# Kernel optimization log

Hardware: AMD Instinct MI355X
Metric: run time of the kernel (lower is better)

The kernel has to match this reference:

```python
import jax, jax.numpy as jnp
import numpy as np

N_EMBED = 1024
N_HEADS = 16


def setup_inputs() -> dict:
    key = jax.random.key(0)
    k_x, k_wa, k_wp = jax.random.split(key, 3)
    B, T, C = 2, 2048, N_EMBED
    x = jax.random.normal(k_x, (B, T, C), dtype=jnp.float32)
    # flax Dense default: lecun_normal kernel, zero bias; use scaled normal here
    w_attn = jax.random.normal(k_wa, (C, 3 * C), dtype=jnp.float32) / np.sqrt(C)
    b_attn = jnp.zeros((3 * C,), dtype=jnp.float32)
    w_proj = jax.random.normal(k_wp, (C, C), dtype=jnp.float32) / np.sqrt(C)
    b_proj = jnp.zeros((C,), dtype=jnp.float32)
    return {"x": x, "w_attn": w_attn, "b_attn": b_attn,
            "w_proj": w_proj, "b_proj": b_proj}


def reference(x, w_attn, b_attn, w_proj, b_proj):
    B, T, C = x.shape
    H = N_HEADS
    D = C // H
    qkv = x @ w_attn + b_attn                      # [B,T,3C]
    q, k, v = jnp.split(qkv, 3, axis=-1)           # each [B,T,C]
    q = q.reshape(B, T, H, D).swapaxes(1, 2)       # [B,H,T,D]
    k = k.reshape(B, T, H, D).swapaxes(1, 2)
    v = v.reshape(B, T, H, D).swapaxes(1, 2)
    att = jnp.einsum('bhid,bhjd->bhij', q, k) * (1.0 / jnp.sqrt(D))
    causal = jnp.tril(jnp.ones((T, T), dtype=bool))
    att = jnp.where(causal, att, -jnp.inf)
    att = jax.nn.softmax(att, axis=-1)
    y = jnp.einsum('bhij,bhjd->bhid', att, v)      # [B,H,T,D]
    y = y.swapaxes(1, 2).reshape(B, T, C)
    return y @ w_proj + b_proj
```

## Files before the change

kernel.cpp:

```cpp
#include <hip/hip_runtime.h>
#include <hip/hip_bf16.h>

typedef __bf16 bf16x8 __attribute__((ext_vector_type(8)));
typedef float f32x4 __attribute__((ext_vector_type(4)));
typedef float f32x16 __attribute__((ext_vector_type(16)));
typedef unsigned short u16;
typedef unsigned int u32;
typedef u16 u16x8 __attribute__((ext_vector_type(8)));
typedef u32 u32x4 __attribute__((ext_vector_type(4)));

#define SM_SCALE 0.1803368801111244f

#define FEXP2(x) __builtin_amdgcn_exp2f(x)
#define FLOG2(x) __builtin_amdgcn_logf(x)

__device__ inline u16 tobf(float f) {
  u32 u = __builtin_bit_cast(u32, f);
  u32 r = (u + 0x7fffu + ((u >> 16) & 1u)) >> 16;
  return (u16)r;
}

__device__ inline float frombf(u16 h) {
  return __builtin_bit_cast(float, (u32)h << 16);
}

__device__ inline void gload_lds16(const void* g, void* lds) {
  __builtin_amdgcn_global_load_lds(
      (const __attribute__((address_space(1))) u32*)g,
      (__attribute__((address_space(3))) u32*)lds, 16, 0, 0);
}

template <int N>
__device__ __forceinline__ void wait_vmcnt() {
  if constexpr (N == 0)
    asm volatile("s_waitcnt vmcnt(0)" ::: "memory");
  else if constexpr (N == 5)
    asm volatile("s_waitcnt vmcnt(5)" ::: "memory");
  else if constexpr (N == 7)
    asm volatile("s_waitcnt vmcnt(7)" ::: "memory");
}

__device__ __forceinline__ void transpose_body(const float* __restrict__ in,
                                               u16* __restrict__ out, int K,
                                               int N, int bxg, int tid) {
  __shared__ float tile[32][33];
  int nbx = N >> 5;
  int bx = bxg % nbx, by = bxg / nbx;
  int k0 = by << 5, n0 = bx << 5;
  int tx = tid & 31, ty = tid >> 5;
#pragma unroll
  for (int j = 0; j < 4; ++j) {
    int row = ty + j * 8;
    tile[row][tx] = in[(size_t)(k0 + row) * N + n0 + tx];
  }
  __syncthreads();
#pragma unroll
  for (int j = 0; j < 4; ++j) {
    int row = ty + j * 8;
    out[(size_t)(n0 + row) * K + k0 + tx] = tobf(tile[tx][row]);
  }
}

__global__ __launch_bounds__(256) void prep_kernel(
    const float* __restrict__ x, u16* __restrict__ xb,
    const float* __restrict__ wa, u16* __restrict__ wat,
    const float* __restrict__ wp, u16* __restrict__ wpt) {
  const int b = blockIdx.x, tid = threadIdx.x;
  if (b < 2048) {
    int i = b * 256 + tid;
    const float4* p = (const float4*)x + (size_t)i * 2;
    float4 a = p[0], c = p[1];
    u16x8 v;
    v[0] = tobf(a.x); v[1] = tobf(a.y); v[2] = tobf(a.z); v[3] = tobf(a.w);
    v[4] = tobf(c.x); v[5] = tobf(c.y); v[6] = tobf(c.z); v[7] = tobf(c.w);
    *(u16x8*)(xb + (size_t)i * 8) = v;
  } else if (b < 5120) {
    transpose_body(wa, wat, 1024, 3072, b - 2048, tid);
  } else {
    transpose_body(wp, wpt, 1024, 1024, b - 5120, tid);
  }
}

template <int EPI, int BN>
__global__ __launch_bounds__(256) void gemm_bt(
    const u16* __restrict__ A, const u16* __restrict__ Bt,
    const float* __restrict__ bias,
    u16* __restrict__ o0, u16* __restrict__ o1, u16* __restrict__ o2,
    float* __restrict__ fo, int M, int N, int K) {
  constexpr int NF = BN / 32;
  __shared__ __align__(16) u16 As[2][128 * 64];
  __shared__ __align__(16) u16 Bs[2][BN * 64];
  const int tid = threadIdx.x;
  const int lane = tid & 63;
  const int wave = tid >> 6;
  const int nbn = N / BN;
  int bid = (int)blockIdx.x;
  const int cpx = (int)gridDim.x >> 3;
  bid = (bid & 7) * cpx + (bid >> 3);
  const int bm = bid / nbn, bn = bid % nbn;
  const int m0 = bm << 7, n0 = bn * BN;
  const int wr = wave >> 1, wc = wave & 1;
  const int r15 = lane & 15, g = lane >> 4;

  f32x4 acc[4][NF] = {};

#define GSTAGE(buf, kt)                                                    \
  do {                                                                     \
    _Pragma("unroll")                                                      \
    for (int j = 0; j < 4; ++j) {                                          \
      int c = j * 4 + wave;                                                \
      int byte0 = c * 1024 + lane * 16;                                    \
      int row = byte0 >> 7;                                                \
      int colb = (byte0 & 127) ^ ((row & 7) << 4);                         \
      gload_lds16(A + (size_t)(m0 + row) * K + (kt) * 64 + (colb >> 1),    \
                  (char*)As[(buf)] + c * 1024);                            \
    }                                                                      \
    _Pragma("unroll")                                                      \
    for (int j = 0; j < NF; ++j) {                                         \
      int c = j * 4 + wave;                                                \
      int byte0 = c * 1024 + lane * 16;                                    \
      int row = byte0 >> 7;                                                \
      int colb = (byte0 & 127) ^ ((row & 7) << 4);                         \
      gload_lds16(Bt + (size_t)(n0 + row) * K + (kt) * 64 + (colb >> 1),   \
                  (char*)Bs[(buf)] + c * 1024);                            \
    }                                                                      \
  } while (0)

  const int nkt = K >> 6;
  GSTAGE(0, 0);
  for (int kt = 0; kt < nkt; ++kt) {
    const int cur = kt & 1;
    if (kt + 1 < nkt) {
      GSTAGE(cur ^ 1, kt + 1);
      wait_vmcnt<4 + NF>();
    } else {
      wait_vmcnt<0>();
    }
    __builtin_amdgcn_s_barrier();
#pragma unroll
    for (int kk = 0; kk < 2; ++kk) {
      bf16x8 af[4], bf[NF];
#pragma unroll
      for (int i = 0; i < 4; ++i) {
        int rowA = wr * 64 + i * 16 + r15;
        int ca = (kk * 64 + 16 * g) ^ ((rowA & 7) << 4);
        af[i] = *(const bf16x8*)((const char*)As[cur] + rowA * 128 + ca);
      }
#pragma unroll
      for (int j2 = 0; j2 < NF; ++j2) {
        int rowB = wc * (BN / 2) + j2 * 16 + r15;
        int cb = (kk * 64 + 16 * g) ^ ((rowB & 7) << 4);
        bf[j2] = *(const bf16x8*)((const char*)Bs[cur] + rowB * 128 + cb);
      }
#pragma unroll
      for (int i = 0; i < 4; ++i)
#pragma unroll
        for (int j2 = 0; j2 < NF; ++j2)
          acc[i][j2] = __builtin_amdgcn_mfma_f32_16x16x32_bf16(
              af[i], bf[j2], acc[i][j2], 0, 0, 0);
    }
    if (kt + 1 < nkt) __builtin_amdgcn_s_barrier();
  }
#undef GSTAGE

#pragma unroll
  for (int j2 = 0; j2 < NF; ++j2) {
    const int n = n0 + wc * (BN / 2) + j2 * 16 + r15;
    const float bv = bias[n];
#pragma unroll
    for (int i = 0; i < 4; ++i) {
      const int mb = m0 + wr * 64 + i * 16 + g * 4;
      float v[4];
#pragma unroll
      for (int rr = 0; rr < 4; ++rr) v[rr] = acc[i][j2][rr] + bv;
      if (EPI == 1) {
#pragma unroll
        for (int rr = 0; rr < 4; ++rr) fo[(size_t)(mb + rr) * N + n] = v[rr];
      } else {
        const int b = mb >> 11, t = mb & 2047;
        const int sec = n >> 10, nn = n & 1023;
        const int h = nn >> 6, d = nn & 63;
        const int bh = b * 16 + h;
        if (sec == 0) {
          u16* base = o0 + ((size_t)bh * 2048 + t) * 64 + d;
#pragma unroll
          for (int rr = 0; rr < 4; ++rr) base[rr * 64] = tobf(v[rr] * SM_SCALE);
        } else if (sec == 1) {
          u16* kb = o1 +
                    (((size_t)(bh * 32 + (t >> 6)) * 4 + (d >> 4)) * 2) * 512 +
                    ((d >> 3) & 1) * 256 + (d & 7);
          const int tb = t & 63;
#pragma unroll
          for (int rr = 0; rr < 4; ++rr) {
            int r = tb + rr;
            kb[(r >> 5) * 512 + (r & 31) * 8] = tobf(v[rr]);
          }
        } else {
          const int tl = t & 63;
          u16* vb = o2 +
                    ((((size_t)(bh * 32 + (t >> 6)) * 4 + (tl >> 4)) * 2 +
                      (d >> 5)) * 512) +
                    ((tl >> 3) & 1) * 256 + (d & 31) * 8 + (tl & 7);
          u32* p = (u32*)vb;
          p[0] = (u32)tobf(v[0]) | ((u32)tobf(v[1]) << 16);
          p[1] = (u32)tobf(v[2]) | ((u32)tobf(v[3]) << 16);
        }
      }
    }
  }
}

static __device__ const signed char PT_C[34] =
    {15,15,15,15,14,14,14,13,13,13,12,12,12,11,11,11,10,10,10,9,9,8,8,7,7,6,6,5,5,4,3,2,1,0};
static __device__ const signed char PT_K0[34] =
    {0,8,16,24,0,10,20,0,9,18,0,8,17,0,8,16,0,7,14,0,10,0,9,0,8,0,7,0,6,0,0,0,0,0};
static __device__ const signed char PT_KN[34] =
    {8,16,24,32,10,20,30,9,18,28,8,17,26,8,16,24,7,14,22,10,20,9,18,8,16,7,14,6,12,10,8,6,4,2};
static __device__ const signed char PT_SL[34] =
    {-1,0,1,2,-1,3,4,-1,5,6,-1,7,8,-1,9,10,-1,11,12,-1,13,-1,14,-1,15,-1,16,-1,17,-2,-2,-2,-2,-2};

__global__ __launch_bounds__(256) void attn_kernel(
    const u16* __restrict__ qb, const u16* __restrict__ kpk,
    const u16* __restrict__ vpk, u16* __restrict__ yb,
    u16* __restrict__ party, float* __restrict__ partM) {
  const int tid = threadIdx.x;
  const int lane = tid & 63;
  const int w = tid >> 6;
  const int q31 = lane & 31, hi = lane >> 5;
  const int bx = blockIdx.x;
  const int pid = bx >> 5, bh = bx & 31;
  const int c = PT_C[pid];
  const int kt0 = PT_K0[pid], ktN = PT_KN[pid];
  const int slot = PT_SL[pid];

  const int q0 = c * 128 + w * 32;
  const int qg = q0 + q31;
  const int qmax = q0 + 31;
  const int ktEnd = min(ktN, (qmax >> 6) + 1);

  const u16* qrow = qb + ((size_t)bh * 2048 + qg) * 64;
  bf16x8 aq[4];
#pragma unroll
  for (int ks = 0; ks < 4; ++ks)
    aq[ks] = *(const bf16x8*)(qrow + ks * 16 + 8 * hi);

  f32x16 o0 = {}, o1 = {};
  float m = -INFINITY, l = 0.f;

  const u16* kbh = kpk + (size_t)bh * 32 * 4096 + lane * 8;
  const u16* vbh = vpk + (size_t)bh * 32 * 4096 + lane * 8;

  for (int kt = kt0; kt < ktEnd; ++kt) {
    const u16* kp = kbh + (size_t)kt * 4096;
    const u16* vp = vbh + (size_t)kt * 4096;

    bf16x8 kf[8];
#pragma unroll
    for (int j = 0; j < 8; ++j) kf[j] = *(const bf16x8*)(kp + j * 512);

    f32x16 s0 = {}, s1 = {};
    __builtin_amdgcn_s_setprio(1);
#pragma unroll
    for (int ks = 0; ks < 4; ++ks) {
      s0 = __builtin_amdgcn_mfma_f32_32x32x16_bf16(kf[2 * ks], aq[ks], s0, 0, 0, 0);
      s1 = __builtin_amdgcn_mfma_f32_32x32x16_bf16(kf[2 * ks + 1], aq[ks], s1, 0, 0, 0);
    }
    __builtin_amdgcn_s_setprio(0);

    if (kt * 64 + 63 > q0) {
      const int thr = qg - kt * 64;
#pragma unroll
      for (int r = 0; r < 16; ++r) {
        const int off = (r & 3) + 8 * (r >> 2) + 4 * hi;
        if (off > thr) s0[r] = -INFINITY;
        if (off + 32 > thr) s1[r] = -INFINITY;
      }
    }
    f32x16 mx;
#pragma unroll
    for (int r = 0; r < 16; ++r) mx[r] = fmaxf(s0[r], s1[r]);
#pragma unroll
    for (int st = 8; st >= 1; st >>= 1)
#pragma unroll
      for (int r = 0; r < st; ++r) mx[r] = fmaxf(mx[r], mx[r + st]);
    float mt = fmaxf(mx[0], __shfl_xor(mx[0], 32, 64));

    if (kt == kt0) {
      m = mt;
    } else if (__any(mt > m + 8.f)) {
      float mnew = fmaxf(m, mt);
      float alpha = FEXP2(m - mnew);
      m = mnew;
      l *= alpha;
#pragma unroll
      for (int r = 0; r < 16; ++r) {
        o0[r] *= alpha;
        o1[r] *= alpha;
      }
    }
#pragma unroll
    for (int r = 0; r < 16; ++r) {
      s0[r] = FEXP2(s0[r] - m);
      s1[r] = FEXP2(s1[r] - m);
    }
    {
      float la = 0.f, lb = 0.f, lc2 = 0.f, ld = 0.f;
#pragma unroll
      for (int r = 0; r < 16; r += 2) {
        la += s0[r];
        lb += s0[r + 1];
        lc2 += s1[r];
        ld += s1[r + 1];
      }
      l += (la + lb) + (lc2 + ld);
    }
    u32 W[16];
#pragma unroll
    for (int i2 = 0; i2 < 8; ++i2) {
      asm("v_cvt_pk_bf16_f32 %0, %1, %2"
          : "=v"(W[i2]) : "v"(s0[2 * i2]), "v"(s0[2 * i2 + 1]));
      asm("v_cvt_pk_bf16_f32 %0, %1, %2"
          : "=v"(W[8 + i2]) : "v"(s1[2 * i2]), "v"(s1[2 * i2 + 1]));
    }
#pragma unroll
    for (int b4 = 0; b4 < 16; b4 += 4) {
      asm("v_permlane32_swap_b32 %0, %1" : "+v"(W[b4]), "+v"(W[b4 + 2]));
      asm("v_permlane32_swap_b32 %0, %1" : "+v"(W[b4 + 1]), "+v"(W[b4 + 3]));
    }
    bf16x8 vf[8];
#pragma unroll
    for (int j = 0; j < 8; ++j) vf[j] = *(const bf16x8*)(vp + j * 512);

    __builtin_amdgcn_s_setprio(1);
#pragma unroll
    for (int ks = 0; ks < 4; ++ks) {
      u32x4 pwv = {W[4 * ks], W[4 * ks + 1], W[4 * ks + 2], W[4 * ks + 3]};
      bf16x8 pf = __builtin_bit_cast(bf16x8, pwv);
      o0 = __builtin_amdgcn_mfma_f32_32x32x16_bf16(vf[2 * ks], pf, o0, 0, 0, 0);
      o1 = __builtin_amdgcn_mfma_f32_32x32x16_bf16(vf[2 * ks + 1], pf, o1, 0, 0, 0);
    }
    __builtin_amdgcn_s_setprio(0);
  }

  l += __shfl_xor(l, 32, 64);
  float inv = 1.0f / l;

  u32* dst;
  if (slot >= 0) {
    dst = (u32*)(party +
                 ((size_t)((slot * 32 + bh) * 128 + w * 32 + q31)) * 64);
  } else {
    int b = bh >> 4, hd = bh & 15;
    dst = (u32*)(yb + ((size_t)b * 2048 + qg) * 1024 + hd * 64);
  }
#pragma unroll
  for (int r = 0; r < 16; r += 2) {
    int d = (r & 3) + 8 * (r >> 2) + 4 * hi;
    dst[d >> 1] = (u32)tobf(o0[r] * inv) | ((u32)tobf(o0[r + 1] * inv) << 16);
    dst[(d + 32) >> 1] =
        (u32)tobf(o1[r] * inv) | ((u32)tobf(o1[r + 1] * inv) << 16);
  }
  if (slot != -2 && hi == 0)
    partM[(pid * 32 + bh) * 128 + w * 32 + q31] = m + FLOG2(l);
}

static __device__ const signed char CB_PID[11] = {0,4,7,10,13,16,19,21,23,25,27};
static __device__ const signed char CB_P[11]   = {4,3,3,3,3,3,2,2,2,2,2};
static __device__ const signed char CB_SL[11]  = {0,3,5,7,9,11,13,14,15,16,17};

__global__ __launch_bounds__(256) void attn_combine(
    const u16* __restrict__ party, const float* __restrict__ partM,
    u16* __restrict__ yb) {
  const int gi = blockIdx.x;
  const int ci = gi >> 5, bh = gi & 31;
  const int c = 15 - ci;
  const int pidb = CB_PID[ci], P = CB_P[ci], slb = CB_SL[ci];
  const int row = threadIdx.x >> 1, off = (threadIdx.x & 1) * 32;

  const float M0 = partM[((pidb + 0) * 32 + bh) * 128 + row];
  const float M1 = partM[((pidb + 1) * 32 + bh) * 128 + row];
  const float M2 = (P > 2) ? partM[((pidb + 2) * 32 + bh) * 128 + row] : -INFINITY;
  const float M3 = (P > 3) ? partM[((pidb + 3) * 32 + bh) * 128 + row] : -INFINITY;
  const float Mm = fmaxf(fmaxf(M0, M1), fmaxf(M2, M3));
  const float w0 = FEXP2(M0 - Mm), w1 = FEXP2(M1 - Mm);
  const float w2 = FEXP2(M2 - Mm), w3 = FEXP2(M3 - Mm);
  const float inv = 1.f / (w0 + w1 + w2 + w3);

  const int b = bh >> 4, head = bh & 15, t = c * 128 + row;
  u16* y = yb + ((size_t)b * 2048 + t) * 1024 + head * 64 + off;

  float acc[32];
#pragma unroll
  for (int j = 0; j < 4; ++j) {
    u16x8 a = *(const u16x8*)(y + j * 8);
#pragma unroll
    for (int e = 0; e < 8; ++e) acc[j * 8 + e] = frombf(a[e]) * w0;
  }
  {
    const u16* p1 = party + ((size_t)((slb + 0) * 32 + bh) * 128 + row) * 64 + off;
#pragma unroll
    for (int j = 0; j < 4; ++j) {
      u16x8 a = *(const u16x8*)(p1 + j * 8);
#pragma unroll
      for (int e = 0; e < 8; ++e) acc[j * 8 + e] += frombf(a[e]) * w1;
    }
  }
  if (P > 2) {
    const u16* p2 = party + ((size_t)((slb + 1) * 32 + bh) * 128 + row) * 64 + off;
#pragma unroll
    for (int j = 0; j < 4; ++j) {
      u16x8 a = *(const u16x8*)(p2 + j * 8);
#pragma unroll
      for (int e = 0; e < 8; ++e) acc[j * 8 + e] += frombf(a[e]) * w2;
    }
  }
  if (P > 3) {
    const u16* p3 = party + ((size_t)((slb + 2) * 32 + bh) * 128 + row) * 64 + off;
#pragma unroll
    for (int j = 0; j < 4; ++j) {
      u16x8 a = *(const u16x8*)(p3 + j * 8);
#pragma unroll
      for (int e = 0; e < 8; ++e) acc[j * 8 + e] += frombf(a[e]) * w3;
    }
  }
#pragma unroll
  for (int j = 0; j < 4; ++j) {
    u16x8 ov;
#pragma unroll
    for (int e = 0; e < 8; ++e) ov[e] = tobf(acc[j * 8 + e] * inv);
    *(u16x8*)(y + j * 8) = ov;
  }
}

extern "C" void kernel_launch(void* const* d_in, const int* in_sizes, int n_in,
                              void* d_out, int out_size, void* d_ws,
                              size_t ws_size, hipStream_t stream) {
  const float* x = (const float*)d_in[0];
  const float* w_attn = (const float*)d_in[1];
  const float* b_attn = (const float*)d_in[2];
  const float* w_proj = (const float*)d_in[3];
  const float* b_proj = (const float*)d_in[4];
  float* out = (float*)d_out;
  char* ws = (char*)d_ws;

  u16* xb = (u16*)ws;
  u16* wat = (u16*)(ws + (8ull << 20));
  u16* wpt = (u16*)(ws + (14ull << 20));
  u16* qbuf = (u16*)(ws + (16ull << 20));
  u16* kpk = (u16*)(ws + (24ull << 20));
  u16* vpk = (u16*)(ws + (32ull << 20));
  u16* yb = (u16*)(ws + (40ull << 20));
  u16* party = (u16*)ws;
  float* partM = (float*)(ws + (10ull << 20));

  prep_kernel<<<6144, 256, 0, stream>>>(x, xb, w_attn, wat, w_proj, wpt);
  gemm_bt<0, 192><<<32 * 16, 256, 0, stream>>>(xb, wat, b_attn, qbuf, kpk,
                                               vpk, nullptr, 4096, 3072, 1024);
  attn_kernel<<<34 * 32, 256, 0, stream>>>(qbuf, kpk, vpk, yb, party, partM);
  attn_combine<<<352, 256, 0, stream>>>(party, partM, yb);
  gemm_bt<1, 64><<<32 * 16, 256, 0, stream>>>(yb, wpt, b_proj, nullptr,
                                              nullptr, nullptr, out, 4096,
                                              1024, 1024);
}
```

Before: 103.8 us.

## Split KV tiles across waves within a block and combine partials in LDS

Each attention block now owns 32 query rows instead of 128, and its four waves stride over the key/value tiles. The waves merge their partial softmax states (max, sum, output) through shared memory before writing. This replaces the cross-block split-K tables, the global partial buffers and the separate combine kernel, removing one launch and the global round trip for partials. In exchange it uses about 35 KB of LDS per block and adds a block barrier. Low-query blocks leave most waves idle, since a wave with no tile contributes a zero partial.

```diff
diff --git a/kernel.cpp b/kernel.cpp
--- a/kernel.cpp
+++ b/kernel.cpp
@@ -12,16 +12,11 @@
 #define SM_SCALE 0.1803368801111244f
 
 #define FEXP2(x) __builtin_amdgcn_exp2f(x)
-#define FLOG2(x) __builtin_amdgcn_logf(x)
 
 __device__ inline u16 tobf(float f) {
   u32 u = __builtin_bit_cast(u32, f);
   u32 r = (u + 0x7fffu + ((u >> 16) & 1u)) >> 16;
   return (u16)r;
-}
-
-__device__ inline float frombf(u16 h) {
-  return __builtin_bit_cast(float, (u32)h << 16);
 }
 
 __device__ inline void gload_lds16(const void* g, void* lds) {
@@ -210,33 +205,21 @@
   }
 }
 
-static __device__ const signed char PT_C[34] =
-    {15,15,15,15,14,14,14,13,13,13,12,12,12,11,11,11,10,10,10,9,9,8,8,7,7,6,6,5,5,4,3,2,1,0};
-static __device__ const signed char PT_K0[34] =
-    {0,8,16,24,0,10,20,0,9,18,0,8,17,0,8,16,0,7,14,0,10,0,9,0,8,0,7,0,6,0,0,0,0,0};
-static __device__ const signed char PT_KN[34] =
-    {8,16,24,32,10,20,30,9,18,28,8,17,26,8,16,24,7,14,22,10,20,9,18,8,16,7,14,6,12,10,8,6,4,2};
-static __device__ const signed char PT_SL[34] =
-    {-1,0,1,2,-1,3,4,-1,5,6,-1,7,8,-1,9,10,-1,11,12,-1,13,-1,14,-1,15,-1,16,-1,17,-2,-2,-2,-2,-2};
-
 __global__ __launch_bounds__(256) void attn_kernel(
     const u16* __restrict__ qb, const u16* __restrict__ kpk,
-    const u16* __restrict__ vpk, u16* __restrict__ yb,
-    u16* __restrict__ party, float* __restrict__ partM) {
+    const u16* __restrict__ vpk, u16* __restrict__ yb) {
+  __shared__ float Of[4][32 * 67];
+  __shared__ float Ml[4][32], Ll[4][32];
   const int tid = threadIdx.x;
   const int lane = tid & 63;
-  const int w = tid >> 6;
+  const int kw = tid >> 6;
   const int q31 = lane & 31, hi = lane >> 5;
   const int bx = blockIdx.x;
-  const int pid = bx >> 5, bh = bx & 31;
-  const int c = PT_C[pid];
-  const int kt0 = PT_K0[pid], ktN = PT_KN[pid];
-  const int slot = PT_SL[pid];
-
-  const int q0 = c * 128 + w * 32;
+  const int cq = 63 - (bx >> 5);
+  const int bh = bx & 31;
+  const int q0 = cq * 32;
   const int qg = q0 + q31;
-  const int qmax = q0 + 31;
-  const int ktEnd = min(ktN, (qmax >> 6) + 1);
+  const int ktEnd = ((q0 + 31) >> 6) + 1;
 
   const u16* qrow = qb + ((size_t)bh * 2048 + qg) * 64;
   bf16x8 aq[4];
@@ -250,7 +233,7 @@
   const u16* kbh = kpk + (size_t)bh * 32 * 4096 + lane * 8;
   const u16* vbh = vpk + (size_t)bh * 32 * 4096 + lane * 8;
 
-  for (int kt = kt0; kt < ktEnd; ++kt) {
+  for (int kt = kw; kt < ktEnd; kt += 4) {
     const u16* kp = kbh + (size_t)kt * 4096;
     const u16* vp = vbh + (size_t)kt * 4096;
 
@@ -285,7 +268,7 @@
       for (int r = 0; r < st; ++r) mx[r] = fmaxf(mx[r], mx[r + st]);
     float mt = fmaxf(mx[0], __shfl_xor(mx[0], 32, 64));
 
-    if (kt == kt0) {
+    if (kt == kw) {
       m = mt;
     } else if (__any(mt > m + 8.f)) {
       float mnew = fmaxf(m, mt);
@@ -343,92 +326,37 @@
   }
 
   l += __shfl_xor(l, 32, 64);
-  float inv = 1.0f / l;
-
-  u32* dst;
-  if (slot >= 0) {
-    dst = (u32*)(party +
-                 ((size_t)((slot * 32 + bh) * 128 + w * 32 + q31)) * 64);
-  } else {
-    int b = bh >> 4, hd = bh & 15;
-    dst = (u32*)(yb + ((size_t)b * 2048 + qg) * 1024 + hd * 64);
-  }
-#pragma unroll
-  for (int r = 0; r < 16; r += 2) {
-    int d = (r & 3) + 8 * (r >> 2) + 4 * hi;
-    dst[d >> 1] = (u32)tobf(o0[r] * inv) | ((u32)tobf(o0[r + 1] * inv) << 16);
-    dst[(d + 32) >> 1] =
-        (u32)tobf(o1[r] * inv) | ((u32)tobf(o1[r + 1] * inv) << 16);
-  }
-  if (slot != -2 && hi == 0)
-    partM[(pid * 32 + bh) * 128 + w * 32 + q31] = m + FLOG2(l);
-}
-
-static __device__ const signed char CB_PID[11] = {0,4,7,10,13,16,19,21,23,25,27};
-static __device__ const signed char CB_P[11]   = {4,3,3,3,3,3,2,2,2,2,2};
-static __device__ const signed char CB_SL[11]  = {0,3,5,7,9,11,13,14,15,16,17};
-
-__global__ __launch_bounds__(256) void attn_combine(
-    const u16* __restrict__ party, const float* __restrict__ partM,
-    u16* __restrict__ yb) {
-  const int gi = blockIdx.x;
-  const int ci = gi >> 5, bh = gi & 31;
-  const int c = 15 - ci;
-  const int pidb = CB_PID[ci], P = CB_P[ci], slb = CB_SL[ci];
-  const int row = threadIdx.x >> 1, off = (threadIdx.x & 1) * 32;
-
-  const float M0 = partM[((pidb + 0) * 32 + bh) * 128 + row];
-  const float M1 = partM[((pidb + 1) * 32 + bh) * 128 + row];
-  const float M2 = (P > 2) ? partM[((pidb + 2) * 32 + bh) * 128 + row] : -INFINITY;
-  const float M3 = (P > 3) ? partM[((pidb + 3) * 32 + bh) * 128 + row] : -INFINITY;
-  const float Mm = fmaxf(fmaxf(M0, M1), fmaxf(M2, M3));
-  const float w0 = FEXP2(M0 - Mm), w1 = FEXP2(M1 - Mm);
-  const float w2 = FEXP2(M2 - Mm), w3 = FEXP2(M3 - Mm);
-  const float inv = 1.f / (w0 + w1 + w2 + w3);
-
-  const int b = bh >> 4, head = bh & 15, t = c * 128 + row;
-  u16* y = yb + ((size_t)b * 2048 + t) * 1024 + head * 64 + off;
-
-  float acc[32];
-#pragma unroll
-  for (int j = 0; j < 4; ++j) {
-    u16x8 a = *(const u16x8*)(y + j * 8);
-#pragma unroll
-    for (int e = 0; e < 8; ++e) acc[j * 8 + e] = frombf(a[e]) * w0;
-  }
-  {
-    const u16* p1 = party + ((size_t)((slb + 0) * 32 + bh) * 128 + row) * 64 + off;
-#pragma unroll
-    for (int j = 0; j < 4; ++j) {
-      u16x8 a = *(const u16x8*)(p1 + j * 8);
-#pragma unroll
-      for (int e = 0; e < 8; ++e) acc[j * 8 + e] += frombf(a[e]) * w1;
-    }
-  }
-  if (P > 2) {
-    const u16* p2 = party + ((size_t)((slb + 1) * 32 + bh) * 128 + row) * 64 + off;
-#pragma unroll
-    for (int j = 0; j < 4; ++j) {
-      u16x8 a = *(const u16x8*)(p2 + j * 8);
-#pragma unroll
-      for (int e = 0; e < 8; ++e) acc[j * 8 + e] += frombf(a[e]) * w2;
-    }
-  }
-  if (P > 3) {
-    const u16* p3 = party + ((size_t)((slb + 2) * 32 + bh) * 128 + row) * 64 + off;
-#pragma unroll
-    for (int j = 0; j < 4; ++j) {
-      u16x8 a = *(const u16x8*)(p3 + j * 8);
-#pragma unroll
-      for (int e = 0; e < 8; ++e) acc[j * 8 + e] += frombf(a[e]) * w3;
-    }
-  }
-#pragma unroll
-  for (int j = 0; j < 4; ++j) {
-    u16x8 ov;
-#pragma unroll
-    for (int e = 0; e < 8; ++e) ov[e] = tobf(acc[j * 8 + e] * inv);
-    *(u16x8*)(y + j * 8) = ov;
+
+  float* OfW = &Of[kw][0];
+#pragma unroll
+  for (int r = 0; r < 16; ++r) {
+    const int d = (r & 3) + 8 * (r >> 2) + 4 * hi;
+    OfW[q31 * 67 + d] = o0[r];
+    OfW[q31 * 67 + d + 32] = o1[r];
+  }
+  if (hi == 0) {
+    Ml[kw][q31] = m;
+    Ll[kw][q31] = l;
+  }
+  __syncthreads();
+
+  const int q = tid >> 3, d0 = (tid & 7) * 8;
+  const float m0 = Ml[0][q], m1 = Ml[1][q], m2 = Ml[2][q], m3 = Ml[3][q];
+  const float Mx = fmaxf(fmaxf(m0, m1), fmaxf(m2, m3));
+  const float w0 = FEXP2(m0 - Mx), w1 = FEXP2(m1 - Mx);
+  const float w2 = FEXP2(m2 - Mx), w3 = FEXP2(m3 - Mx);
+  const float L = w0 * Ll[0][q] + w1 * Ll[1][q] + w2 * Ll[2][q] + w3 * Ll[3][q];
+  const float inv = 1.0f / L;
+  const int b = bh >> 4, hd = bh & 15;
+  u32* dst = (u32*)(yb + ((size_t)b * 2048 + q0 + q) * 1024 + hd * 64 + d0);
+  const int base = q * 67 + d0;
+#pragma unroll
+  for (int e = 0; e < 8; e += 2) {
+    float v0 = (Of[0][base + e] * w0 + Of[1][base + e] * w1 +
+                Of[2][base + e] * w2 + Of[3][base + e] * w3) * inv;
+    float v1 = (Of[0][base + e + 1] * w0 + Of[1][base + e + 1] * w1 +
+                Of[2][base + e + 1] * w2 + Of[3][base + e + 1] * w3) * inv;
+    dst[e >> 1] = (u32)tobf(v0) | ((u32)tobf(v1) << 16);
   }
 }
 
@@ -450,14 +378,11 @@
   u16* kpk = (u16*)(ws + (24ull << 20));
   u16* vpk = (u16*)(ws + (32ull << 20));
   u16* yb = (u16*)(ws + (40ull << 20));
-  u16* party = (u16*)ws;
-  float* partM = (float*)(ws + (10ull << 20));
 
   prep_kernel<<<6144, 256, 0, stream>>>(x, xb, w_attn, wat, w_proj, wpt);
   gemm_bt<0, 192><<<32 * 16, 256, 0, stream>>>(xb, wat, b_attn, qbuf, kpk,
                                                vpk, nullptr, 4096, 3072, 1024);
-  attn_kernel<<<34 * 32, 256, 0, stream>>>(qbuf, kpk, vpk, yb, party, partM);
-  attn_combine<<<352, 256, 0, stream>>>(party, partM, yb);
+  attn_kernel<<<2048, 256, 0, stream>>>(qbuf, kpk, vpk, yb);
   gemm_bt<1, 64><<<32 * 16, 256, 0, stream>>>(yb, wpt, b_proj, nullptr,
                                               nullptr, nullptr, out, 4096,
                                               1024, 1024);
```

After: 97.96 us (median of 3 runs). -5.6%, faster.
